# Optimization experiments

Measured on AMD Instinct MI355X. Metric: run time of the kernel, lower is better.

## Reference

```python
import jax, jax.numpy as jnp
import numpy as np

N, F, H, C, E = 100000, 128, 128, 32, 600000


def setup_inputs() -> dict:
    key = jax.random.key(0)
    ks = jax.random.split(key, 8)
    x = jax.random.normal(ks[0], (N, F), dtype=jnp.float32)
    edge_index = jax.random.randint(ks[1], (2, E), 0, N, dtype=jnp.int64)
    s = 1.0 / np.sqrt(F)
    sh = 1.0 / np.sqrt(H)
    W1l = jax.random.uniform(ks[2], (F, H), jnp.float32, -s, s)
    W1r = jax.random.uniform(ks[3], (F, H), jnp.float32, -s, s)
    b1 = jnp.zeros((H,), jnp.float32)
    W2l = jax.random.uniform(ks[4], (H, C), jnp.float32, -sh, sh)
    W2r = jax.random.uniform(ks[5], (H, C), jnp.float32, -sh, sh)
    b2 = jnp.zeros((C,), jnp.float32)
    return {"x": x, "edge_index": edge_index, "W1l": W1l, "b1": b1,
            "W1r": W1r, "W2l": W2l, "b2": b2, "W2r": W2r}


def reference(x, edge_index, W1l, b1, W1r, W2l, b2, W2r):
    # PyG SAGEConv: out = lin_l(mean_{j in N(i)} x_j) + lin_r(x_i)
    # (lin_l has bias, lin_r does not). Dropout is identity in eval mode.
    src, dst = edge_index[0], edge_index[1]
    n = x.shape[0]
    deg = jax.ops.segment_sum(jnp.ones((src.shape[0],), x.dtype), dst, num_segments=n)
    inv_deg = 1.0 / jnp.maximum(deg, 1.0)  # clamp: isolated nodes get 0 agg

    def sage(h, Wl, bl, Wr):
        agg = jax.ops.segment_sum(h[src], dst, num_segments=n)  # [N, d] gather+scatter
        agg = agg * inv_deg[:, None]
        return agg @ Wl + bl + h @ Wr

    h = jax.nn.relu(sage(x, W1l, b1, W1r))
    return sage(h, W2l, b2, W2r)
```

## Files before the change

### kernel.cpp

```cpp
#include <hip/hip_runtime.h>
#include <hip/hip_bf16.h>


#define FDIM 128
#define CDIM 32
#define SCAN_CHUNK 1024
#define PSTR 136

typedef __attribute__((ext_vector_type(8))) short short8;
typedef __attribute__((ext_vector_type(4))) float f32x4;
typedef unsigned short ushort_t;
typedef unsigned int uint_t;

static __device__ __forceinline__ ushort_t f2bf(float f) {
    uint_t u = __float_as_uint(f);
    u += 0x7fffu + ((u >> 16) & 1u);
    return (ushort_t)(u >> 16);
}
static __device__ __forceinline__ float bf2f_lo(uint_t u) {
    return __uint_as_float(u << 16);
}
static __device__ __forceinline__ float bf2f_hi(uint_t u) {
    return __uint_as_float(u & 0xffff0000u);
}


__global__ __launch_bounds__(256) void prep_kernel(
        const int* __restrict__ dst, int* __restrict__ deg, int E, int n,
        const float* __restrict__ x, uint_t* __restrict__ xb4, long long total8,
        const float* __restrict__ W1l, const float* __restrict__ W1r,
        const float* __restrict__ W2l, const float* __restrict__ W2r,
        ushort_t* __restrict__ w1lt, ushort_t* __restrict__ w1rt,
        ushort_t* __restrict__ w2lt, ushort_t* __restrict__ w2rt,
        int DB4, int CB) {
    int b = (int)blockIdx.x;
    if (b < DB4) {
        int e0 = (b * 256 + threadIdx.x) * 4;
        if (e0 + 3 < E) {
            int4 d4 = *(const int4*)(dst + e0);
            if (d4.x >= 0 && d4.x < n) atomicAdd(&deg[d4.x], 1);
            if (d4.y >= 0 && d4.y < n) atomicAdd(&deg[d4.y], 1);
            if (d4.z >= 0 && d4.z < n) atomicAdd(&deg[d4.z], 1);
            if (d4.w >= 0 && d4.w < n) atomicAdd(&deg[d4.w], 1);
        } else {
            for (int e = e0; e < E; e++) {
                int d = dst[e];
                if (d >= 0 && d < n) atomicAdd(&deg[d], 1);
            }
        }
    } else if (b < DB4 + CB) {
        long long i = (long long)(b - DB4) * 256 + threadIdx.x;
        if (i >= total8) return;
        const float4* p = (const float4*)x + i * 2;
        float4 v0 = p[0], v1 = p[1];
        uint4 o;
        o.x = (uint_t)f2bf(v0.x) | ((uint_t)f2bf(v0.y) << 16);
        o.y = (uint_t)f2bf(v0.z) | ((uint_t)f2bf(v0.w) << 16);
        o.z = (uint_t)f2bf(v1.x) | ((uint_t)f2bf(v1.y) << 16);
        o.w = (uint_t)f2bf(v1.z) | ((uint_t)f2bf(v1.w) << 16);
        ((uint4*)xb4)[i] = o;
    } else {
        int idx = (b - DB4 - CB) * 256 + threadIdx.x;
        const float* w; ushort_t* wt; int Nc, local;
        if (idx < 16384)      { w = W1l; wt = w1lt; Nc = 128; local = idx; }
        else if (idx < 32768) { w = W1r; wt = w1rt; Nc = 128; local = idx - 16384; }
        else if (idx < 36864) { w = W2l; wt = w2lt; Nc = 32;  local = idx - 32768; }
        else if (idx < 40960) { w = W2r; wt = w2rt; Nc = 32;  local = idx - 36864; }
        else return;
        int nn = local >> 7, kk = local & 127;
        wt[nn * 128 + kk] = f2bf(w[kk * Nc + nn]);
    }
}


__global__ __launch_bounds__(256) void scan1_kernel(
        const int* __restrict__ deg, int* __restrict__ partials, int n) {
    __shared__ int red[256];
    int t = threadIdx.x;
    int base = blockIdx.x * SCAN_CHUNK + t * 4;
    int s = 0;
    if (base + 3 < n) {
        int4 v = *(const int4*)(deg + base);
        s = v.x + v.y + v.z + v.w;
    } else {
        for (int i = 0; i < 4; i++) if (base + i < n) s += deg[base + i];
    }
    red[t] = s;
    __syncthreads();
#pragma unroll
    for (int off = 128; off > 0; off >>= 1) {
        if (t < off) red[t] += red[t + off];
        __syncthreads();
    }
    if (t == 0) partials[blockIdx.x] = red[0];
}

__global__ __launch_bounds__(256) void scan3_kernel(
        const int* __restrict__ deg, const int* __restrict__ partials,
        int* __restrict__ rowptr, int* __restrict__ cursor, int n, int SB) {
    __shared__ int s[256];
    int t = threadIdx.x;
    int pre = (t < SB && t < (int)blockIdx.x) ? partials[t] : 0;
    s[t] = pre;
    __syncthreads();
#pragma unroll
    for (int off = 128; off > 0; off >>= 1) {
        if (t < off) s[t] += s[t + off];
        __syncthreads();
    }
    int blockbase = s[0];
    __syncthreads();

    int base = blockIdx.x * SCAN_CHUNK + t * 4;
    int d0 = 0, d1 = 0, d2 = 0, d3 = 0;
    if (base + 3 < n) {
        int4 v = *(const int4*)(deg + base);
        d0 = v.x; d1 = v.y; d2 = v.z; d3 = v.w;
    } else {
        if (base + 0 < n) d0 = deg[base + 0];
        if (base + 1 < n) d1 = deg[base + 1];
        if (base + 2 < n) d2 = deg[base + 2];
        if (base + 3 < n) d3 = deg[base + 3];
    }
    s[t] = d0 + d1 + d2 + d3;
    __syncthreads();
#pragma unroll
    for (int off = 1; off < 256; off <<= 1) {
        int u = (t >= off) ? s[t - off] : 0;
        __syncthreads();
        s[t] += u;
        __syncthreads();
    }
    int run = blockbase + ((t == 0) ? 0 : s[t - 1]);
    int dd[4] = {d0, d1, d2, d3};
#pragma unroll
    for (int i = 0; i < 4; i++) {
        if (base + i < n) {
            rowptr[base + i] = run;
            cursor[base + i] = run;
            run += dd[i];
        }
    }
}


__global__ void fill_kernel(const int* __restrict__ src, const int* __restrict__ dst,
                            int* __restrict__ cursor, int* __restrict__ nbr,
                            int E, int n) {
    int e0 = (blockIdx.x * 256 + threadIdx.x) * 4;
    if (e0 + 3 < E) {
        int4 s4 = *(const int4*)(src + e0);
        int4 d4 = *(const int4*)(dst + e0);
        if (d4.x >= 0 && d4.x < n) { int p = atomicAdd(&cursor[d4.x], 1); nbr[p] = s4.x; }
        if (d4.y >= 0 && d4.y < n) { int p = atomicAdd(&cursor[d4.y], 1); nbr[p] = s4.y; }
        if (d4.z >= 0 && d4.z < n) { int p = atomicAdd(&cursor[d4.z], 1); nbr[p] = s4.z; }
        if (d4.w >= 0 && d4.w < n) { int p = atomicAdd(&cursor[d4.w], 1); nbr[p] = s4.w; }
    } else {
        for (int e = e0; e < E; e++) {
            int d = dst[e];
            if (d >= 0 && d < n) { int p = atomicAdd(&cursor[d], 1); nbr[p] = src[e]; }
        }
    }
}


__global__ __launch_bounds__(256) void agg1_kernel(
        const uint_t* __restrict__ xbu ,
        const int* __restrict__ rowptr, const int* __restrict__ deg,
        const int* __restrict__ nbr, uint_t* __restrict__ aggbu, int n) {
    int t = threadIdx.x;
    int i = blockIdx.x * 16 + (t >> 4);
    if (i >= n) return;
    int l16 = t & 15;
    int start = rowptr[i];
    int d     = deg[i];
    float s[8] = {0.f, 0.f, 0.f, 0.f, 0.f, 0.f, 0.f, 0.f};
    int e = 0;
    for (; e + 1 < d; e += 2) {
        int j0 = nbr[start + e];
        int j1 = nbr[start + e + 1];
        uint4 u0 = *(const uint4*)(xbu + (size_t)j0 * 64 + l16 * 4);
        uint4 u1 = *(const uint4*)(xbu + (size_t)j1 * 64 + l16 * 4);
        s[0] += bf2f_lo(u0.x) + bf2f_lo(u1.x); s[1] += bf2f_hi(u0.x) + bf2f_hi(u1.x);
        s[2] += bf2f_lo(u0.y) + bf2f_lo(u1.y); s[3] += bf2f_hi(u0.y) + bf2f_hi(u1.y);
        s[4] += bf2f_lo(u0.z) + bf2f_lo(u1.z); s[5] += bf2f_hi(u0.z) + bf2f_hi(u1.z);
        s[6] += bf2f_lo(u0.w) + bf2f_lo(u1.w); s[7] += bf2f_hi(u0.w) + bf2f_hi(u1.w);
    }
    if (e < d) {
        int j = nbr[start + e];
        uint4 u = *(const uint4*)(xbu + (size_t)j * 64 + l16 * 4);
        s[0] += bf2f_lo(u.x); s[1] += bf2f_hi(u.x);
        s[2] += bf2f_lo(u.y); s[3] += bf2f_hi(u.y);
        s[4] += bf2f_lo(u.z); s[5] += bf2f_hi(u.z);
        s[6] += bf2f_lo(u.w); s[7] += bf2f_hi(u.w);
    }
    float inv = 1.0f / (float)(d > 0 ? d : 1);
    uint4 o;
    o.x = (uint_t)f2bf(s[0] * inv) | ((uint_t)f2bf(s[1] * inv) << 16);
    o.y = (uint_t)f2bf(s[2] * inv) | ((uint_t)f2bf(s[3] * inv) << 16);
    o.z = (uint_t)f2bf(s[4] * inv) | ((uint_t)f2bf(s[5] * inv) << 16);
    o.w = (uint_t)f2bf(s[6] * inv) | ((uint_t)f2bf(s[7] * inv) << 16);
    *(uint4*)(aggbu + (size_t)i * 64 + l16 * 4) = o;
}


__global__ __launch_bounds__(512, 6) void fused12_kernel(
        const ushort_t* __restrict__ xb, const ushort_t* __restrict__ aggb,
        const ushort_t* __restrict__ w1lt, const ushort_t* __restrict__ w1rt,
        const ushort_t* __restrict__ w2lt, const ushort_t* __restrict__ w2rt,
        const float* __restrict__ b1,
        ushort_t* __restrict__ z2b, float* __restrict__ r2, int n) {
    __shared__ ushort_t xs[64 * PSTR];
    __shared__ ushort_t as_[64 * PSTR];
    __shared__ ushort_t ws2[2 * 32 * PSTR];

    const int t    = threadIdx.x;
    const int wave = t >> 6;
    const int lane = t & 63;
    const int quad = lane >> 4;
    const int l16  = lane & 15;
    const int row0 = blockIdx.x * 64;
    const int c1   = wave * 16;

#pragma unroll
    for (int it = 0; it < 2; it++) {
        int c   = t + it * 512;
        int row = c >> 4, col = c & 15;
        int grow = row0 + row; if (grow >= n) grow = n - 1;
        size_t goff = (size_t)grow * FDIM + col * 8;
        short8 vx = *(const short8*)(xb + goff);
        short8 va = *(const short8*)(aggb + goff);
        *(short8*)(xs  + row * PSTR + col * 8) = vx;
        *(short8*)(as_ + row * PSTR + col * 8) = va;
    }
#pragma unroll
    for (int it = 0; it < 2; it++) {
        int c = t + it * 512;
        int m = c >> 9, lo = c & 511;
        int row = lo >> 4, col = lo & 15;
        const ushort_t* sw = m ? w2rt : w2lt;
        *(short8*)(ws2 + (m * 32 + row) * PSTR + col * 8) =
            *(const short8*)(sw + row * 128 + col * 8);
    }

    short8 bl1[4], br1[4];
#pragma unroll
    for (int k = 0; k < 4; k++) {
        size_t woff = (size_t)(c1 + l16) * FDIM + k * 32 + quad * 8;
        bl1[k] = *(const short8*)(w1lt + woff);
        br1[k] = *(const short8*)(w1rt + woff);
    }
    float b1c = b1[c1 + l16];

    __syncthreads();

    f32x4 acc1[4];
#pragma unroll
    for (int r = 0; r < 4; r++) acc1[r] = (f32x4){0.f, 0.f, 0.f, 0.f};

#pragma unroll
    for (int k = 0; k < 4; k++) {
        short8 a1[4], a2[4];
#pragma unroll
        for (int r = 0; r < 4; r++) {
            int lro = (r * 16 + l16) * PSTR + k * 32 + quad * 8;
            a1[r] = *(const short8*)(as_ + lro);
            a2[r] = *(const short8*)(xs  + lro);
        }
#pragma unroll
        for (int r = 0; r < 4; r++) {
            acc1[r] = __builtin_amdgcn_mfma_f32_16x16x32_bf16(a1[r], bl1[k], acc1[r], 0, 0, 0);
            acc1[r] = __builtin_amdgcn_mfma_f32_16x16x32_bf16(a2[r], br1[k], acc1[r], 0, 0, 0);
        }
    }

    __syncthreads();

    ushort_t* hs = xs;
#pragma unroll
    for (int r = 0; r < 4; r++)
#pragma unroll
        for (int reg = 0; reg < 4; reg++) {
            int lrow = r * 16 + quad * 4 + reg;
            float v = acc1[r][reg] + b1c;
            v = v > 0.f ? v : 0.f;
            hs[lrow * PSTR + c1 + l16] = f2bf(v);
        }

    __syncthreads();

    const int rs = (wave >> 1) * 16;
    const int c2 = (wave & 1) * 16;
    f32x4 a2l = (f32x4){0.f, 0.f, 0.f, 0.f};
    f32x4 a2r = (f32x4){0.f, 0.f, 0.f, 0.f};
#pragma unroll
    for (int k = 0; k < 4; k++) {
        short8 ah = *(const short8*)(hs  + (rs + l16) * PSTR + k * 32 + quad * 8);
        short8 wl = *(const short8*)(ws2 + (c2 + l16) * PSTR + k * 32 + quad * 8);
        short8 wr = *(const short8*)(ws2 + (32 + c2 + l16) * PSTR + k * 32 + quad * 8);
        a2l = __builtin_amdgcn_mfma_f32_16x16x32_bf16(ah, wl, a2l, 0, 0, 0);
        a2r = __builtin_amdgcn_mfma_f32_16x16x32_bf16(ah, wr, a2r, 0, 0, 0);
    }
#pragma unroll
    for (int reg = 0; reg < 4; reg++) {
        int grow = row0 + rs + quad * 4 + reg;
        if (grow < n) {
            z2b[(size_t)grow * CDIM + c2 + l16] = f2bf(a2l[reg]);
            r2 [(size_t)grow * CDIM + c2 + l16] = a2r[reg];
        }
    }
}


__global__ __launch_bounds__(256) void combine2_kernel(
        const uint_t* __restrict__ z2bu ,
        const int* __restrict__ rowptr, const int* __restrict__ deg,
        const int* __restrict__ nbr, const float* __restrict__ b2,
        const float* __restrict__ r2, float* __restrict__ out, int n) {
    int t = threadIdx.x;
    int i = blockIdx.x * 16 + (t >> 4);
    if (i >= n) return;
    int l16 = t & 15;
    int start = rowptr[i];
    int d     = deg[i];
    float s0 = 0.f, s1 = 0.f;
    int e = 0;
    for (; e + 1 < d; e += 2) {
        int j0 = nbr[start + e];
        int j1 = nbr[start + e + 1];
        uint_t u0 = z2bu[(size_t)j0 * 16 + l16];
        uint_t u1 = z2bu[(size_t)j1 * 16 + l16];
        s0 += bf2f_lo(u0) + bf2f_lo(u1);
        s1 += bf2f_hi(u0) + bf2f_hi(u1);
    }
    if (e < d) {
        int j = nbr[start + e];
        uint_t u = z2bu[(size_t)j * 16 + l16];
        s0 += bf2f_lo(u);
        s1 += bf2f_hi(u);
    }
    float inv = 1.0f / (float)(d > 0 ? d : 1);
    float2 rr = *(const float2*)(r2 + (size_t)i * CDIM + l16 * 2);
    float2 bb = *(const float2*)(b2 + l16 * 2);
    float2 o;
    o.x = s0 * inv + rr.x + bb.x;
    o.y = s1 * inv + rr.y + bb.y;
    *(float2*)(out + (size_t)i * CDIM + l16 * 2) = o;
}


extern "C" void kernel_launch(void* const* d_in, const int* in_sizes, int n_in,
                              void* d_out, int out_size, void* d_ws, size_t ws_size,
                              hipStream_t stream) {
    const float* x   = (const float*)d_in[0];
    const int*   ei  = (const int*)d_in[1];
    const float* W1l = (const float*)d_in[2];
    const float* b1  = (const float*)d_in[3];
    const float* W1r = (const float*)d_in[4];
    const float* W2l = (const float*)d_in[5];
    const float* b2  = (const float*)d_in[6];
    const float* W2r = (const float*)d_in[7];

    const int N = in_sizes[0] / FDIM;
    const int E = in_sizes[1] / 2;
    const int* src = ei;
    const int* dst = ei + E;

    char* p = (char*)d_ws;
    int*      deg      = (int*)p;      p += (size_t)N * sizeof(int);
    int*      cursor   = (int*)p;      p += (size_t)N * sizeof(int);
    int*      rowptr   = (int*)p;      p += (size_t)N * sizeof(int);
    int*      partials = (int*)p;      p += 256 * sizeof(int);
    ushort_t* w1lt     = (ushort_t*)p; p += FDIM * FDIM * sizeof(ushort_t);
    ushort_t* w1rt     = (ushort_t*)p; p += FDIM * FDIM * sizeof(ushort_t);
    ushort_t* w2lt     = (ushort_t*)p; p += FDIM * CDIM * sizeof(ushort_t);
    ushort_t* w2rt     = (ushort_t*)p; p += FDIM * CDIM * sizeof(ushort_t);
    int*      nbr      = (int*)p;      p += (size_t)((E + 3) / 4 * 4) * sizeof(int);
    ushort_t* xb       = (ushort_t*)p; p += (size_t)N * FDIM * sizeof(ushort_t);
    ushort_t* aggb     = (ushort_t*)p; p += (size_t)N * FDIM * sizeof(ushort_t);
    ushort_t* z2b      = (ushort_t*)p; p += (size_t)N * CDIM * sizeof(ushort_t);
    float*    r2       = (float*)p;    p += (size_t)N * CDIM * sizeof(float);

    const int SB = (N + SCAN_CHUNK - 1) / SCAN_CHUNK;
    const long long total8 = (long long)N * FDIM / 8;
    const int CB = (int)((total8 + 255) / 256);
    const int E4 = (E + 3) / 4;
    const int DB4 = (E4 + 255) / 256;
    const int WB = (40960 + 255) / 256;

    hipMemsetAsync(deg, 0, (size_t)N * sizeof(int), stream);

    prep_kernel <<<DB4 + CB + WB, 256, 0, stream>>>(dst, deg, E, N,
                                                    x, (uint_t*)xb, total8,
                                                    W1l, W1r, W2l, W2r,
                                                    w1lt, w1rt, w2lt, w2rt, DB4, CB);
    scan1_kernel<<<SB, 256, 0, stream>>>(deg, partials, N);
    scan3_kernel<<<SB, 256, 0, stream>>>(deg, partials, rowptr, cursor, N, SB);
    fill_kernel <<<DB4, 256, 0, stream>>>(src, dst, cursor, nbr, E, N);

    agg1_kernel   <<<(N + 15) / 16, 256, 0, stream>>>((const uint_t*)xb, rowptr, deg, nbr,
                                                      (uint_t*)aggb, N);
    fused12_kernel<<<(N + 63) / 64, 512, 0, stream>>>(xb, aggb, w1lt, w1rt, w2lt, w2rt,
                                                      b1, z2b, r2, N);
    combine2_kernel<<<(N + 15) / 16, 256, 0, stream>>>((const uint_t*)z2b, rowptr, deg, nbr,
                                                       b2, r2, (float*)d_out, N);
}
```

Before: 235.4 us.

## Fuse layer-1 neighbor aggregation into the fused GEMM kernel via shared memory

Removes the separate agg1 kernel and its global bf16 agg buffer. Each fused12 block now gathers and mean-reduces neighbor features for its 64 rows directly into the shared-memory tile the MFMA stage reads. This drops one launch plus the write and re-read of an N×128 bf16 array. In exchange, the irregular gather latency now sits inside a 512-thread block with heavier register and LDS use, which may reduce latency hiding compared with the lightweight standalone gather kernel.

Result: faster. 229.2 us (-2.6%).

```diff
diff --git a/kernel.cpp b/kernel.cpp
--- a/kernel.cpp
+++ b/kernel.cpp
@@ -164,48 +164,10 @@
 }
 
 
-__global__ __launch_bounds__(256) void agg1_kernel(
-        const uint_t* __restrict__ xbu ,
+__global__ __launch_bounds__(512, 6) void fused12_kernel(
+        const ushort_t* __restrict__ xb,
         const int* __restrict__ rowptr, const int* __restrict__ deg,
-        const int* __restrict__ nbr, uint_t* __restrict__ aggbu, int n) {
-    int t = threadIdx.x;
-    int i = blockIdx.x * 16 + (t >> 4);
-    if (i >= n) return;
-    int l16 = t & 15;
-    int start = rowptr[i];
-    int d     = deg[i];
-    float s[8] = {0.f, 0.f, 0.f, 0.f, 0.f, 0.f, 0.f, 0.f};
-    int e = 0;
-    for (; e + 1 < d; e += 2) {
-        int j0 = nbr[start + e];
-        int j1 = nbr[start + e + 1];
-        uint4 u0 = *(const uint4*)(xbu + (size_t)j0 * 64 + l16 * 4);
-        uint4 u1 = *(const uint4*)(xbu + (size_t)j1 * 64 + l16 * 4);
-        s[0] += bf2f_lo(u0.x) + bf2f_lo(u1.x); s[1] += bf2f_hi(u0.x) + bf2f_hi(u1.x);
-        s[2] += bf2f_lo(u0.y) + bf2f_lo(u1.y); s[3] += bf2f_hi(u0.y) + bf2f_hi(u1.y);
-        s[4] += bf2f_lo(u0.z) + bf2f_lo(u1.z); s[5] += bf2f_hi(u0.z) + bf2f_hi(u1.z);
-        s[6] += bf2f_lo(u0.w) + bf2f_lo(u1.w); s[7] += bf2f_hi(u0.w) + bf2f_hi(u1.w);
-    }
-    if (e < d) {
-        int j = nbr[start + e];
-        uint4 u = *(const uint4*)(xbu + (size_t)j * 64 + l16 * 4);
-        s[0] += bf2f_lo(u.x); s[1] += bf2f_hi(u.x);
-        s[2] += bf2f_lo(u.y); s[3] += bf2f_hi(u.y);
-        s[4] += bf2f_lo(u.z); s[5] += bf2f_hi(u.z);
-        s[6] += bf2f_lo(u.w); s[7] += bf2f_hi(u.w);
-    }
-    float inv = 1.0f / (float)(d > 0 ? d : 1);
-    uint4 o;
-    o.x = (uint_t)f2bf(s[0] * inv) | ((uint_t)f2bf(s[1] * inv) << 16);
-    o.y = (uint_t)f2bf(s[2] * inv) | ((uint_t)f2bf(s[3] * inv) << 16);
-    o.z = (uint_t)f2bf(s[4] * inv) | ((uint_t)f2bf(s[5] * inv) << 16);
-    o.w = (uint_t)f2bf(s[6] * inv) | ((uint_t)f2bf(s[7] * inv) << 16);
-    *(uint4*)(aggbu + (size_t)i * 64 + l16 * 4) = o;
-}
-
-
-__global__ __launch_bounds__(512, 6) void fused12_kernel(
-        const ushort_t* __restrict__ xb, const ushort_t* __restrict__ aggb,
+        const int* __restrict__ nbr,
         const ushort_t* __restrict__ w1lt, const ushort_t* __restrict__ w1rt,
         const ushort_t* __restrict__ w2lt, const ushort_t* __restrict__ w2rt,
         const float* __restrict__ b1,
@@ -222,16 +184,15 @@
     const int row0 = blockIdx.x * 64;
     const int c1   = wave * 16;
 
+    const uint_t* xbu = (const uint_t*)xb;
+
 #pragma unroll
     for (int it = 0; it < 2; it++) {
         int c   = t + it * 512;
         int row = c >> 4, col = c & 15;
         int grow = row0 + row; if (grow >= n) grow = n - 1;
         size_t goff = (size_t)grow * FDIM + col * 8;
-        short8 vx = *(const short8*)(xb + goff);
-        short8 va = *(const short8*)(aggb + goff);
-        *(short8*)(xs  + row * PSTR + col * 8) = vx;
-        *(short8*)(as_ + row * PSTR + col * 8) = va;
+        *(short8*)(xs + row * PSTR + col * 8) = *(const short8*)(xb + goff);
     }
 #pragma unroll
     for (int it = 0; it < 2; it++) {
@@ -241,6 +202,41 @@
         const ushort_t* sw = m ? w2rt : w2lt;
         *(short8*)(ws2 + (m * 32 + row) * PSTR + col * 8) =
             *(const short8*)(sw + row * 128 + col * 8);
+    }
+
+    const int grp = t >> 4;
+    for (int rr = 0; rr < 2; rr++) {
+        int row = grp + rr * 32;
+        int i = row0 + row;
+        float s[8] = {0.f, 0.f, 0.f, 0.f, 0.f, 0.f, 0.f, 0.f};
+        int start = 0, d = 0;
+        if (i < n) { start = rowptr[i]; d = deg[i]; }
+        int e = 0;
+        for (; e + 1 < d; e += 2) {
+            int j0 = nbr[start + e];
+            int j1 = nbr[start + e + 1];
+            uint4 u0 = *(const uint4*)(xbu + (size_t)j0 * 64 + l16 * 4);
+            uint4 u1 = *(const uint4*)(xbu + (size_t)j1 * 64 + l16 * 4);
+            s[0] += bf2f_lo(u0.x) + bf2f_lo(u1.x); s[1] += bf2f_hi(u0.x) + bf2f_hi(u1.x);
+            s[2] += bf2f_lo(u0.y) + bf2f_lo(u1.y); s[3] += bf2f_hi(u0.y) + bf2f_hi(u1.y);
+            s[4] += bf2f_lo(u0.z) + bf2f_lo(u1.z); s[5] += bf2f_hi(u0.z) + bf2f_hi(u1.z);
+            s[6] += bf2f_lo(u0.w) + bf2f_lo(u1.w); s[7] += bf2f_hi(u0.w) + bf2f_hi(u1.w);
+        }
+        if (e < d) {
+            int j = nbr[start + e];
+            uint4 u = *(const uint4*)(xbu + (size_t)j * 64 + l16 * 4);
+            s[0] += bf2f_lo(u.x); s[1] += bf2f_hi(u.x);
+            s[2] += bf2f_lo(u.y); s[3] += bf2f_hi(u.y);
+            s[4] += bf2f_lo(u.z); s[5] += bf2f_hi(u.z);
+            s[6] += bf2f_lo(u.w); s[7] += bf2f_hi(u.w);
+        }
+        float inv = 1.0f / (float)(d > 0 ? d : 1);
+        uint4 o;
+        o.x = (uint_t)f2bf(s[0] * inv) | ((uint_t)f2bf(s[1] * inv) << 16);
+        o.y = (uint_t)f2bf(s[2] * inv) | ((uint_t)f2bf(s[3] * inv) << 16);
+        o.z = (uint_t)f2bf(s[4] * inv) | ((uint_t)f2bf(s[5] * inv) << 16);
+        o.w = (uint_t)f2bf(s[6] * inv) | ((uint_t)f2bf(s[7] * inv) << 16);
+        *(uint4*)(as_ + row * PSTR + l16 * 8) = o;
     }
 
     short8 bl1[4], br1[4];
@@ -377,7 +373,6 @@
     ushort_t* w2rt     = (ushort_t*)p; p += FDIM * CDIM * sizeof(ushort_t);
     int*      nbr      = (int*)p;      p += (size_t)((E + 3) / 4 * 4) * sizeof(int);
     ushort_t* xb       = (ushort_t*)p; p += (size_t)N * FDIM * sizeof(ushort_t);
-    ushort_t* aggb     = (ushort_t*)p; p += (size_t)N * FDIM * sizeof(ushort_t);
     ushort_t* z2b      = (ushort_t*)p; p += (size_t)N * CDIM * sizeof(ushort_t);
     float*    r2       = (float*)p;    p += (size_t)N * CDIM * sizeof(float);
 
@@ -398,9 +393,8 @@
     scan3_kernel<<<SB, 256, 0, stream>>>(deg, partials, rowptr, cursor, N, SB);
     fill_kernel <<<DB4, 256, 0, stream>>>(src, dst, cursor, nbr, E, N);
 
-    agg1_kernel   <<<(N + 15) / 16, 256, 0, stream>>>((const uint_t*)xb, rowptr, deg, nbr,
-                                                      (uint_t*)aggb, N);
-    fused12_kernel<<<(N + 63) / 64, 512, 0, stream>>>(xb, aggb, w1lt, w1rt, w2lt, w2rt,
+    fused12_kernel<<<(N + 63) / 64, 512, 0, stream>>>(xb, rowptr, deg, nbr,
+                                                      w1lt, w1rt, w2lt, w2rt,
                                                       b1, z2b, r2, N);
     combine2_kernel<<<(N + 15) / 16, 256, 0, stream>>>((const uint_t*)z2b, rowptr, deg, nbr,
                                                        b2, r2, (float*)d_out, N);
```
